# Performance work log

Hardware: AMD Instinct MI355X
Metric: run time of the kernel (lower is better)

Reference implementation:

```python
import jax, jax.numpy as jnp
import numpy as np

B = 4; C = 768; M = 6; P = 4
VIT = ((32, 32),)                      # ViT token grid (H//16, W//16) for a 512x512 image
PYR = ((64, 64), (32, 32), (16, 16))   # c2/c3/c4 pyramid levels
HID = 192                              # int(768 * cffn_ratio=0.25)


def _ln(x, g, b, eps=1e-6):
    mu = jnp.mean(x, -1, keepdims=True)
    var = jnp.mean((x - mu) ** 2, -1, keepdims=True)
    return (x - mu) * jax.lax.rsqrt(var + eps) * g + b


def _ref_points(shapes):
    # matches get_reference_points: centers of each cell, normalized to [0,1], (x, y) order
    refs = []
    for H, W in shapes:
        gy, gx = jnp.meshgrid((jnp.arange(H) + 0.5) / H, (jnp.arange(W) + 0.5) / W, indexing='ij')
        refs.append(jnp.stack([gx.reshape(-1), gy.reshape(-1)], -1))
    return jnp.concatenate(refs, 0)  # (N, 2)


def _bilinear(v, loc, H, W):
    # v: (B, M, H*W, Dh); loc: (B, Nq, M, P, 2) normalized to [0,1]
    # grid_sample semantics: align_corners=False, zero padding
    Bn, Mn, _, Dh = v.shape
    x = loc[..., 0] * W - 0.5
    y = loc[..., 1] * H - 0.5
    x0 = jnp.floor(x); y0 = jnp.floor(y)
    wx = x - x0; wy = y - y0

    def corner(xi, yi, w):
        valid = ((xi >= 0) & (xi < W) & (yi >= 0) & (yi < H)).astype(v.dtype)
        idx = (jnp.clip(yi, 0, H - 1) * W + jnp.clip(xi, 0, W - 1)).astype(jnp.int32)
        idx = jnp.transpose(idx, (0, 2, 1, 3)).reshape(Bn, Mn, -1)        # (B,M,Nq*P)
        g = jnp.take_along_axis(v, idx[..., None], axis=2)                # (B,M,Nq*P,Dh)
        wt = jnp.transpose(w * valid, (0, 2, 1, 3)).reshape(Bn, Mn, -1)
        return g * wt[..., None]

    return (corner(x0, y0, (1 - wx) * (1 - wy)) + corner(x0 + 1, y0, wx * (1 - wy))
            + corner(x0, y0 + 1, (1 - wx) * wy) + corner(x0 + 1, y0 + 1, wx * wy))


def _msda(q, kv, shapes, ref, ow, ob, aww, awb, vw, vb, pw, pb):
    # Multi-scale deformable attention (MSDeformAttn), proj_ratio=1.0
    Bn, Nq, Cd = q.shape
    L = len(shapes); Dh = Cd // M
    v = kv @ vw + vb                                                      # (B,S,C)
    offs = (q @ ow + ob).reshape(Bn, Nq, M, L, P, 2)
    aw = jax.nn.softmax((q @ aww + awb).reshape(Bn, Nq, M, L * P), -1).reshape(Bn, Nq, M, L, P)
    norm = jnp.asarray([[W, H] for (H, W) in shapes], dtype=q.dtype)      # (L,2), (W,H) order
    locs = ref[None, :, None, None, None, :] + offs / norm[None, None, None, :, None, :]
    out = jnp.zeros((Bn, Nq, M, Dh), q.dtype)
    s = 0
    for l, (H, W) in enumerate(shapes):
        n = H * W
        vl = v[:, s:s + n].reshape(Bn, n, M, Dh).transpose(0, 2, 1, 3)    # (B,M,n,Dh)
        s += n
        g = _bilinear(vl, locs[:, :, :, l], H, W).reshape(Bn, M, Nq, P, Dh)
        out = out + jnp.einsum('bmqpd,bqmp->bqmd', g, aw[:, :, :, l])
    return out.reshape(Bn, Nq, Cd) @ pw + pb


def _conv_ffn(cn, w1, b1, dw, db, w2, b2):
    h = cn @ w1 + b1                                                      # (B,N,HID)
    Bn = cn.shape[0]
    parts = []; s = 0
    for H, W in PYR:
        n = H * W
        seg = h[:, s:s + n].transpose(0, 2, 1).reshape(Bn, HID, H, W)
        seg = jax.lax.conv_general_dilated(seg, dw, (1, 1), 'SAME', feature_group_count=HID)
        seg = seg + db[None, :, None, None]
        parts.append(seg.reshape(Bn, HID, n).transpose(0, 2, 1))
        s += n
    h = jax.nn.gelu(jnp.concatenate(parts, 1), approximate=False)
    return h @ w2 + b2


def setup_inputs() -> dict:
    key = jax.random.key(0)
    ks = iter(jax.random.split(key, 64))

    def rn(*shape, s=0.02):
        return jax.random.normal(next(ks), shape, jnp.float32) * s

    Nvit = 32 * 32
    Npyr = 64 * 64 + 32 * 32 + 16 * 16
    d = {}
    d['x'] = jax.random.normal(next(ks), (B, Nvit, C), jnp.float32)
    d['c'] = jax.random.normal(next(ks), (B, Npyr, C), jnp.float32)
    for pre, L in (('inj', 3), ('ext', 1)):
        d[pre + '_n1g'] = jnp.ones((C,), jnp.float32); d[pre + '_n1b'] = jnp.zeros((C,), jnp.float32)
        d[pre + '_n2g'] = jnp.ones((C,), jnp.float32); d[pre + '_n2b'] = jnp.zeros((C,), jnp.float32)
        d[pre + '_off_w'] = rn(C, M * L * P * 2); d[pre + '_off_b'] = rn(M * L * P * 2, s=0.5)
        d[pre + '_aw_w'] = rn(C, M * L * P); d[pre + '_aw_b'] = jnp.zeros((M * L * P,), jnp.float32)
        d[pre + '_val_w'] = rn(C, C); d[pre + '_val_b'] = jnp.zeros((C,), jnp.float32)
        d[pre + '_out_w'] = rn(C, C); d[pre + '_out_b'] = jnp.zeros((C,), jnp.float32)
    d['inj_gamma'] = rn(C, s=0.1)
    d['ext_ng'] = jnp.ones((C,), jnp.float32); d['ext_nb'] = jnp.zeros((C,), jnp.float32)
    d['ext_fc1_w'] = rn(C, HID); d['ext_fc1_b'] = jnp.zeros((HID,), jnp.float32)
    d['ext_dw_w'] = rn(HID, 1, 3, 3, s=0.1); d['ext_dw_b'] = jnp.zeros((HID,), jnp.float32)
    d['ext_fc2_w'] = rn(HID, C); d['ext_fc2_b'] = jnp.zeros((C,), jnp.float32)
    return d


def reference(x, c, inj_n1g, inj_n1b, inj_n2g, inj_n2b, inj_off_w, inj_off_b, inj_aw_w, inj_aw_b,
              inj_val_w, inj_val_b, inj_out_w, inj_out_b, ext_n1g, ext_n1b, ext_n2g, ext_n2b,
              ext_off_w, ext_off_b, ext_aw_w, ext_aw_b, ext_val_w, ext_val_b, ext_out_w, ext_out_b,
              inj_gamma, ext_ng, ext_nb, ext_fc1_w, ext_fc1_b, ext_dw_w, ext_dw_b, ext_fc2_w, ext_fc2_b):
    ref_inj = _ref_points(VIT)   # queries = ViT tokens, kv = 3-level pyramid
    ref_ext = _ref_points(PYR)   # queries = pyramid tokens, kv = ViT grid (1 level)
    # Injector: x = x + gamma * MSDeformAttn(norm(x), ref, norm(c))
    attn = _msda(_ln(x, inj_n1g, inj_n1b), _ln(c, inj_n2g, inj_n2b), PYR, ref_inj,
                 inj_off_w, inj_off_b, inj_aw_w, inj_aw_b, inj_val_w, inj_val_b, inj_out_w, inj_out_b)
    x = x + inj_gamma * attn
    # Extractor: c = c + MSDeformAttn(norm(c), ref, norm(x)); c = c + ConvFFN(norm(c))
    attn = _msda(_ln(c, ext_n1g, ext_n1b), _ln(x, ext_n2g, ext_n2b), VIT, ref_ext,
                 ext_off_w, ext_off_b, ext_aw_w, ext_aw_b, ext_val_w, ext_val_b, ext_out_w, ext_out_b)
    c = c + attn
    c = c + _conv_ffn(_ln(c, ext_ng, ext_nb), ext_fc1_w, ext_fc1_b, ext_dw_w, ext_dw_b, ext_fc2_w, ext_fc2_b)
    return (x, c)
```

## Files before the change

kernel.cpp:

```cpp
#include <hip/hip_runtime.h>
#include <math.h>
#include <stdint.h>

#define CD 768
#define DH 128
#define MH 6

using half_t = _Float16;
typedef __attribute__((ext_vector_type(8))) _Float16 f16x8;
typedef __attribute__((ext_vector_type(4))) float f32x4;

__device__ __forceinline__ void gload16(const half_t* g, half_t* l) {
  __builtin_amdgcn_global_load_lds((__attribute__((address_space(1))) void*)g,
                                   (__attribute__((address_space(3))) void*)l, 16, 0, 0);
}

static __device__ __forceinline__ float wred(float v) {
#pragma unroll
  for (int off = 32; off > 0; off >>= 1) v += __shfl_down(v, off, 64);
  return v;
}

__global__ __launch_bounds__(256) void ln_f16(const float* __restrict__ in,
                                              const float* __restrict__ g,
                                              const float* __restrict__ b,
                                              half_t* __restrict__ out) {
  int row = blockIdx.x;
  const float* xp = in + (size_t)row * CD;
  half_t* op = out + (size_t)row * CD;
  int t = threadIdx.x;
  float v0 = xp[t], v1 = xp[t + 256], v2 = xp[t + 512];
  __shared__ float wsum[4];
  __shared__ float stat[2];
  int wid = t >> 6, lane = t & 63;
  float s = wred(v0 + v1 + v2);
  if (lane == 0) wsum[wid] = s;
  __syncthreads();
  if (t == 0) stat[0] = (wsum[0] + wsum[1] + wsum[2] + wsum[3]) * (1.0f / 768.0f);
  __syncthreads();
  float mu = stat[0];
  float d0 = v0 - mu, d1 = v1 - mu, d2 = v2 - mu;
  float q = wred(d0 * d0 + d1 * d1 + d2 * d2);
  if (lane == 0) wsum[wid] = q;
  __syncthreads();
  if (t == 0) {
    float var = (wsum[0] + wsum[1] + wsum[2] + wsum[3]) * (1.0f / 768.0f);
    stat[1] = 1.0f / sqrtf(var + 1e-6f);
  }
  __syncthreads();
  float rstd = stat[1];
  op[t]       = (half_t)(d0 * rstd * g[t]       + b[t]);
  op[t + 256] = (half_t)(d1 * rstd * g[t + 256] + b[t + 256]);
  op[t + 512] = (half_t)(d2 * rstd * g[t + 512] + b[t + 512]);
}

__global__ __launch_bounds__(256) void ln_dual(const float* __restrict__ in,
                                               const float* __restrict__ g1,
                                               const float* __restrict__ b1,
                                               half_t* __restrict__ o1,
                                               const float* __restrict__ g2,
                                               const float* __restrict__ b2,
                                               half_t* __restrict__ o2) {
  int row = blockIdx.x;
  const float* xp = in + (size_t)row * CD;
  int t = threadIdx.x;
  float v0 = xp[t], v1 = xp[t + 256], v2 = xp[t + 512];
  __shared__ float wsum[4];
  __shared__ float stat[2];
  int wid = t >> 6, lane = t & 63;
  float s = wred(v0 + v1 + v2);
  if (lane == 0) wsum[wid] = s;
  __syncthreads();
  if (t == 0) stat[0] = (wsum[0] + wsum[1] + wsum[2] + wsum[3]) * (1.0f / 768.0f);
  __syncthreads();
  float mu = stat[0];
  float d0 = v0 - mu, d1 = v1 - mu, d2 = v2 - mu;
  float q = wred(d0 * d0 + d1 * d1 + d2 * d2);
  if (lane == 0) wsum[wid] = q;
  __syncthreads();
  if (t == 0) {
    float var = (wsum[0] + wsum[1] + wsum[2] + wsum[3]) * (1.0f / 768.0f);
    stat[1] = 1.0f / sqrtf(var + 1e-6f);
  }
  __syncthreads();
  float rstd = stat[1];
  half_t* p1 = o1 + (size_t)row * CD;
  half_t* p2 = o2 + (size_t)row * CD;
  float n0 = d0 * rstd, n1 = d1 * rstd, n2 = d2 * rstd;
  p1[t]       = (half_t)(n0 * g1[t]       + b1[t]);
  p1[t + 256] = (half_t)(n1 * g1[t + 256] + b1[t + 256]);
  p1[t + 512] = (half_t)(n2 * g1[t + 512] + b1[t + 512]);
  p2[t]       = (half_t)(n0 * g2[t]       + b2[t]);
  p2[t + 256] = (half_t)(n1 * g2[t + 256] + b2[t + 256]);
  p2[t + 512] = (half_t)(n2 * g2[t + 512] + b2[t + 512]);
}

struct ConvArgs {
  const float* W[10];
  half_t* Wt[10];
  int K[10];
  int N[10];
  int base[11];
};
__global__ __launch_bounds__(256) void convert_all(ConvArgs a) {
  int idx = blockIdx.x * 256 + threadIdx.x;
  if (idx >= a.base[10]) return;
  int s = 0;
  while (idx >= a.base[s + 1]) ++s;
  int local = idx - a.base[s];
  int K = a.K[s], N = a.N[s];
  int n = local / K, k = local - n * K;
  a.Wt[s][local] = (n < N) ? (half_t)a.W[s][(size_t)k * N + n] : (half_t)0.0f;
}

template <int MODE, int OUTF16>
__global__ __launch_bounds__(256) void gemm_mfma(const half_t* __restrict__ A,
                                                 const half_t* __restrict__ Wt,
                                                 const float* __restrict__ bias,
                                                 const float* __restrict__ res,
                                                 const float* __restrict__ gamma,
                                                 void* __restrict__ outv,
                                                 int M, int N, int K) {
  __shared__ half_t smem[8192];
  const int tid = threadIdx.x;
  const int w = tid >> 6;
  const int l = tid & 63;
  const int wr = w >> 1, wc = w & 1;
  const int bm = blockIdx.y * 128;
  const int bn = blockIdx.x * 128;

  f32x4 acc[4][4];
#pragma unroll
  for (int i = 0; i < 4; ++i)
#pragma unroll
    for (int j = 0; j < 4; ++j) acc[i][j] = (f32x4){0.f, 0.f, 0.f, 0.f};

  const int j0 = w * 2;
  const int sr = l >> 2;
  const int sc = (l & 3) * 8;
  const half_t* Ag0 = A + (size_t)(bm + j0 * 16 + sr) * K + sc;
  const half_t* Ag1 = Ag0 + (size_t)16 * K;
  const half_t* Bg0 = Wt + (size_t)(bn + j0 * 16 + sr) * K + sc;
  const half_t* Bg1 = Bg0 + (size_t)16 * K;
  half_t* As0 = smem + j0 * 512;
  half_t* As1 = As0 + 512;
  half_t* Bs0 = smem + 4096 + j0 * 512;
  half_t* Bs1 = Bs0 + 512;

  const int fr = l & 15;
  const int fk = (l >> 4) * 8;
  const int abase = (wr * 64 + fr) * 32 + fk;
  const int bbase = 4096 + (wc * 64 + fr) * 32 + fk;

  for (int k0 = 0; k0 < K; k0 += 32) {
    gload16(Ag0 + k0, As0);
    gload16(Ag1 + k0, As1);
    gload16(Bg0 + k0, Bs0);
    gload16(Bg1 + k0, Bs1);
    __syncthreads();
    f16x8 af[4], bf[4];
#pragma unroll
    for (int i = 0; i < 4; ++i) {
      af[i] = *(const f16x8*)&smem[abase + i * 512];
      bf[i] = *(const f16x8*)&smem[bbase + i * 512];
    }
#pragma unroll
    for (int i = 0; i < 4; ++i)
#pragma unroll
      for (int j = 0; j < 4; ++j)
        acc[i][j] = __builtin_amdgcn_mfma_f32_16x16x32_f16(af[i], bf[j], acc[i][j], 0, 0, 0);
    __syncthreads();
  }

#pragma unroll
  for (int i = 0; i < 4; ++i) {
    int row0 = bm + wr * 64 + i * 16 + (l >> 4) * 4;
#pragma unroll
    for (int r = 0; r < 4; ++r) {
      size_t rowoff = (size_t)(row0 + r) * N;
#pragma unroll
      for (int j = 0; j < 4; ++j) {
        int col = bn + wc * 64 + j * 16 + fr;
        if (col < N) {
          float v = acc[i][j][r] + bias[col];
          if (MODE == 1) v = res[rowoff + col] + gamma[col] * v;
          else if (MODE == 2) v = res[rowoff + col] + v;
          if (OUTF16) ((half_t*)outv)[rowoff + col] = (half_t)v;
          else ((float*)outv)[rowoff + col] = v;
        }
      }
    }
  }
}

__global__ void softmax_lp(float* __restrict__ a, int total, int LP) {
  int i = blockIdx.x * blockDim.x + threadIdx.x;
  if (i >= total) return;
  float* p = a + (size_t)i * LP;
  float mx = -1e30f;
  for (int j = 0; j < LP; ++j) mx = fmaxf(mx, p[j]);
  float s = 0.0f;
  for (int j = 0; j < LP; ++j) {
    float e = expf(p[j] - mx);
    p[j] = e;
    s += e;
  }
  float inv = 1.0f / s;
  for (int j = 0; j < LP; ++j) p[j] *= inv;
}

__global__ __launch_bounds__(256) void sample_inj2(const half_t* __restrict__ v,
                                                   const float* __restrict__ offs,
                                                   const float* __restrict__ aw,
                                                   half_t* __restrict__ out) {
  int tid = threadIdx.x;
  int gp = blockIdx.x * 16 + (tid >> 4);
  int lane16 = tid & 15;
  int m = gp % MH;
  int bq = gp / MH;
  int q = bq & 1023;
  int b = bq >> 10;
  float refx = ((q & 31) + 0.5f) * (1.0f / 32.0f);
  float refy = ((q >> 5) + 0.5f) * (1.0f / 32.0f);
  const float* op = offs + (size_t)gp * 24;
  const float* ap = aw + (size_t)gp * 12;
  const half_t* vb = v + (size_t)b * 5376 * CD + m * DH + lane16 * 8;
  const int Hs[3] = {64, 32, 16};
  const int Ss[3] = {0, 4096, 5120};
  float accf[8];
#pragma unroll
  for (int i = 0; i < 8; ++i) accf[i] = 0.f;
#pragma unroll
  for (int lvl = 0; lvl < 3; ++lvl) {
    int H = Hs[lvl];
    float fH = (float)H;
    const half_t* vl = vb + (size_t)Ss[lvl] * CD;
#pragma unroll
    for (int p = 0; p < 4; ++p) {
      float xx = refx * fH + op[(lvl * 4 + p) * 2 + 0] - 0.5f;
      float yy = refy * fH + op[(lvl * 4 + p) * 2 + 1] - 0.5f;
      float x0f = floorf(xx), y0f = floorf(yy);
      float wx = xx - x0f, wy = yy - y0f;
      int x0 = (int)x0f, y0 = (int)y0f;
      float a = ap[lvl * 4 + p];
      f16x8 acch = (f16x8)(half_t)0.0f;
#pragma unroll
      for (int cy = 0; cy < 2; ++cy)
#pragma unroll
        for (int cx = 0; cx < 2; ++cx) {
          int xi = x0 + cx, yi = y0 + cy;
          bool valid = (xi >= 0) & (xi < H) & (yi >= 0) & (yi < H);
          float wgt = (cx ? wx : 1.f - wx) * (cy ? wy : 1.f - wy) * a;
          int xs = min(max(xi, 0), H - 1), ys = min(max(yi, 0), H - 1);
          half_t wch = (half_t)(valid ? wgt : 0.f);
          f16x8 vv = *(const f16x8*)(vl + (size_t)(ys * H + xs) * CD);
          acch += vv * wch;
        }
#pragma unroll
      for (int i = 0; i < 8; ++i) accf[i] += (float)acch[i];
    }
  }
  f16x8 r;
#pragma unroll
  for (int i = 0; i < 8; ++i) r[i] = (half_t)accf[i];
  *(f16x8*)(out + (size_t)bq * CD + m * DH + lane16 * 8) = r;
}

__global__ __launch_bounds__(256) void sample_ext2(const half_t* __restrict__ v,
                                                   const float* __restrict__ offs,
                                                   const float* __restrict__ aw,
                                                   half_t* __restrict__ out) {
  int tid = threadIdx.x;
  int gp = blockIdx.x * 16 + (tid >> 4);
  int lane16 = tid & 15;
  int m = gp % MH;
  int bq = gp / MH;
  int q = bq % 5376;
  int b = bq / 5376;
  float refx, refy;
  if (q < 4096) {
    refx = ((q & 63) + 0.5f) * (1.0f / 64.0f);
    refy = ((q >> 6) + 0.5f) * (1.0f / 64.0f);
  } else if (q < 5120) {
    int li = q - 4096;
    refx = ((li & 31) + 0.5f) * (1.0f / 32.0f);
    refy = ((li >> 5) + 0.5f) * (1.0f / 32.0f);
  } else {
    int li = q - 5120;
    refx = ((li & 15) + 0.5f) * (1.0f / 16.0f);
    refy = ((li >> 4) + 0.5f) * (1.0f / 16.0f);
  }
  const float* op = offs + (size_t)gp * 8;
  const float* ap = aw + (size_t)gp * 4;
  const half_t* vb = v + (size_t)b * 1024 * CD + m * DH + lane16 * 8;
  float accf[8];
#pragma unroll
  for (int i = 0; i < 8; ++i) accf[i] = 0.f;
#pragma unroll
  for (int p = 0; p < 4; ++p) {
    float xx = refx * 32.0f + op[p * 2 + 0] - 0.5f;
    float yy = refy * 32.0f + op[p * 2 + 1] - 0.5f;
    float x0f = floorf(xx), y0f = floorf(yy);
    float wx = xx - x0f, wy = yy - y0f;
    int x0 = (int)x0f, y0 = (int)y0f;
    float a = ap[p];
    f16x8 acch = (f16x8)(half_t)0.0f;
#pragma unroll
    for (int cy = 0; cy < 2; ++cy)
#pragma unroll
      for (int cx = 0; cx < 2; ++cx) {
        int xi = x0 + cx, yi = y0 + cy;
        bool valid = (xi >= 0) & (xi < 32) & (yi >= 0) & (yi < 32);
        float wgt = (cx ? wx : 1.f - wx) * (cy ? wy : 1.f - wy) * a;
        int xs = min(max(xi, 0), 31), ys = min(max(yi, 0), 31);
        half_t wch = (half_t)(valid ? wgt : 0.f);
        f16x8 vv = *(const f16x8*)(vb + (size_t)(ys * 32 + xs) * CD);
        acch += vv * wch;
      }
#pragma unroll
    for (int i = 0; i < 8; ++i) accf[i] += (float)acch[i];
  }
  f16x8 r;
#pragma unroll
  for (int i = 0; i < 8; ++i) r[i] = (half_t)accf[i];
  *(f16x8*)(out + (size_t)bq * CD + m * DH + lane16 * 8) = r;
}

__global__ __launch_bounds__(192) void dwconv_gelu(const half_t* __restrict__ h,
                                                   const float* __restrict__ w,
                                                   const float* __restrict__ bias,
                                                   half_t* __restrict__ out) {
  int bt = blockIdx.x;
  int tok = bt % 5376;
  int b = bt / 5376;
  int c = threadIdx.x;
  int H, s, li;
  if (tok < 4096) { H = 64; s = 0; li = tok; }
  else if (tok < 5120) { H = 32; s = 4096; li = tok - 4096; }
  else { H = 16; s = 5120; li = tok - 5120; }
  int y = li / H, x = li % H;
  const half_t* hb = h + ((size_t)b * 5376 + s) * 192 + c;
  float acc = 0.0f;
#pragma unroll
  for (int dy = -1; dy <= 1; ++dy) {
    int yy = y + dy;
    if (yy < 0 || yy >= H) continue;
#pragma unroll
    for (int dx = -1; dx <= 1; ++dx) {
      int xx = x + dx;
      if (xx < 0 || xx >= H) continue;
      acc += w[c * 9 + (dy + 1) * 3 + (dx + 1)] * (float)hb[(size_t)(yy * H + xx) * 192];
    }
  }
  acc += bias[c];
  float g = 0.5f * acc * (1.0f + erff(acc * 0.70710678118654752f));
  out[((size_t)b * 5376 + tok) * 192 + c] = (half_t)g;
}

extern "C" void kernel_launch(void* const* d_in, const int* in_sizes, int n_in,
                              void* d_out, int out_size, void* d_ws, size_t ws_size,
                              hipStream_t stream) {
  (void)in_sizes; (void)n_in; (void)out_size; (void)ws_size;
  const float* x        = (const float*)d_in[0];
  const float* c        = (const float*)d_in[1];
  const float* inj_n1g  = (const float*)d_in[2];
  const float* inj_n1b  = (const float*)d_in[3];
  const float* inj_n2g  = (const float*)d_in[4];
  const float* inj_n2b  = (const float*)d_in[5];
  const float* inj_off_w = (const float*)d_in[6];
  const float* inj_off_b = (const float*)d_in[7];
  const float* inj_aw_w = (const float*)d_in[8];
  const float* inj_aw_b = (const float*)d_in[9];
  const float* inj_val_w = (const float*)d_in[10];
  const float* inj_val_b = (const float*)d_in[11];
  const float* inj_out_w = (const float*)d_in[12];
  const float* inj_out_b = (const float*)d_in[13];
  const float* ext_n1g  = (const float*)d_in[14];
  const float* ext_n1b  = (const float*)d_in[15];
  const float* ext_n2g  = (const float*)d_in[16];
  const float* ext_n2b  = (const float*)d_in[17];
  const float* ext_off_w = (const float*)d_in[18];
  const float* ext_off_b = (const float*)d_in[19];
  const float* ext_aw_w = (const float*)d_in[20];
  const float* ext_aw_b = (const float*)d_in[21];
  const float* ext_val_w = (const float*)d_in[22];
  const float* ext_val_b = (const float*)d_in[23];
  const float* ext_out_w = (const float*)d_in[24];
  const float* ext_out_b = (const float*)d_in[25];
  const float* inj_gamma = (const float*)d_in[26];
  const float* ext_ng   = (const float*)d_in[27];
  const float* ext_nb   = (const float*)d_in[28];
  const float* ext_fc1_w = (const float*)d_in[29];
  const float* ext_fc1_b = (const float*)d_in[30];
  const float* ext_dw_w = (const float*)d_in[31];
  const float* ext_dw_b = (const float*)d_in[32];
  const float* ext_fc2_w = (const float*)d_in[33];
  const float* ext_fc2_b = (const float*)d_in[34];

  const int Sx = 4096;
  const int Sc = 21504;
  float* xout = (float*)d_out;
  float* cout = (float*)d_out + (size_t)Sx * CD;

  half_t* bigA   = (half_t*)d_ws;
  half_t* bigA2  = bigA + 16515072;
  half_t* bigV   = bigA2 + 16515072;
  half_t* smallA = bigV + 16515072;
  half_t* smallB = smallA + 3145728;
  half_t* h16    = smallB + 3145728;
  half_t* h2     = h16 + 4128768;
  half_t* w_inj_val = h2 + 4128768;
  half_t* w_inj_out = w_inj_val + 589824;
  half_t* w_ext_val = w_inj_out + 589824;
  half_t* w_ext_out = w_ext_val + 589824;
  half_t* w_fc2     = w_ext_out + 589824;
  half_t* w_inj_off = w_fc2 + 147456;
  half_t* w_inj_aw  = w_inj_off + 196608;
  half_t* w_ext_off = w_inj_aw + 98304;
  half_t* w_ext_aw  = w_ext_off + 98304;
  half_t* w_fc1     = w_ext_aw + 98304;
  float* offsb = (float*)(((uintptr_t)(w_fc1 + 196608) + 255) & ~(uintptr_t)255);
  float* awb = offsb + 1032192;

  ConvArgs ca;
  const float* srcs[10] = {inj_val_w, inj_off_w, inj_aw_w, inj_out_w, ext_val_w,
                           ext_off_w, ext_aw_w, ext_out_w, ext_fc1_w, ext_fc2_w};
  half_t* dsts[10] = {w_inj_val, w_inj_off, w_inj_aw, w_inj_out, w_ext_val,
                      w_ext_off, w_ext_aw, w_ext_out, w_fc1, w_fc2};
  int Ks[10]    = {768, 768, 768, 768, 768, 768, 768, 768, 768, 192};
  int Ns[10]    = {768, 144, 72, 768, 768, 48, 24, 768, 192, 768};
  int Npads[10] = {768, 256, 128, 768, 768, 128, 128, 768, 256, 768};
  int base = 0;
  for (int i = 0; i < 10; ++i) {
    ca.W[i] = srcs[i]; ca.Wt[i] = dsts[i]; ca.K[i] = Ks[i]; ca.N[i] = Ns[i];
    ca.base[i] = base; base += Npads[i] * Ks[i];
  }
  ca.base[10] = base;
  convert_all<<<(base + 255) / 256, 256, 0, stream>>>(ca);

  ln_f16<<<Sx, 256, 0, stream>>>(x, inj_n1g, inj_n1b, smallA);
  ln_dual<<<Sc, 256, 0, stream>>>(c, inj_n2g, inj_n2b, bigA, ext_n1g, ext_n1b, bigA2);
  gemm_mfma<0, 1><<<dim3(6, 168), 256, 0, stream>>>(bigA, w_inj_val, inj_val_b, nullptr, nullptr, bigV, Sc, 768, 768);
  gemm_mfma<0, 0><<<dim3(2, 32), 256, 0, stream>>>(smallA, w_inj_off, inj_off_b, nullptr, nullptr, offsb, Sx, 144, 768);
  gemm_mfma<0, 0><<<dim3(1, 32), 256, 0, stream>>>(smallA, w_inj_aw, inj_aw_b, nullptr, nullptr, awb, Sx, 72, 768);
  softmax_lp<<<(Sx * MH + 255) / 256, 256, 0, stream>>>(awb, Sx * MH, 12);
  sample_inj2<<<(Sx * MH) / 16, 256, 0, stream>>>(bigV, offsb, awb, smallB);
  gemm_mfma<1, 0><<<dim3(6, 32), 256, 0, stream>>>(smallB, w_inj_out, inj_out_b, x, inj_gamma, xout, Sx, 768, 768);

  ln_f16<<<Sx, 256, 0, stream>>>(xout, ext_n2g, ext_n2b, smallA);
  gemm_mfma<0, 1><<<dim3(6, 32), 256, 0, stream>>>(smallA, w_ext_val, ext_val_b, nullptr, nullptr, smallB, Sx, 768, 768);
  gemm_mfma<0, 0><<<dim3(1, 168), 256, 0, stream>>>(bigA2, w_ext_off, ext_off_b, nullptr, nullptr, offsb, Sc, 48, 768);
  gemm_mfma<0, 0><<<dim3(1, 168), 256, 0, stream>>>(bigA2, w_ext_aw, ext_aw_b, nullptr, nullptr, awb, Sc, 24, 768);
  softmax_lp<<<(Sc * MH + 255) / 256, 256, 0, stream>>>(awb, Sc * MH, 4);
  sample_ext2<<<(Sc * MH) / 16, 256, 0, stream>>>(smallB, offsb, awb, bigV);
  gemm_mfma<2, 0><<<dim3(6, 168), 256, 0, stream>>>(bigV, w_ext_out, ext_out_b, c, nullptr, cout, Sc, 768, 768);

  ln_f16<<<Sc, 256, 0, stream>>>(cout, ext_ng, ext_nb, bigA);
  gemm_mfma<0, 1><<<dim3(2, 168), 256, 0, stream>>>(bigA, w_fc1, ext_fc1_b, nullptr, nullptr, h16, Sc, 192, 768);
  dwconv_gelu<<<Sc, 192, 0, stream>>>(h16, ext_dw_w, ext_dw_b, h2);
  gemm_mfma<2, 0><<<dim3(6, 168), 256, 0, stream>>>(h2, w_fc2, ext_fc2_b, cout, nullptr, cout, Sc, 768, 192);
}
```

Measured before the change: 780.0 us.

## Double-buffer GEMM LDS loads, add XCD-aware tile swizzle, vectorize dwconv

The MFMA GEMM now uses two LDS buffers, issuing the next K-tile's global-to-LDS loads before computing on the current tile, so load latency can overlap with MFMA work. Workgroup indices are remapped so that blocks landing on the same XCD process contiguous output tiles, which is meant to improve L2 reuse. The depthwise conv+GELU kernel now processes 8 channels per thread with 16-byte vector loads and stores. The cost is doubled LDS use per block, which may reduce occupancy.

```diff
diff --git a/kernel.cpp b/kernel.cpp
--- a/kernel.cpp
+++ b/kernel.cpp
@@ -121,13 +121,19 @@
                                                  const float* __restrict__ gamma,
                                                  void* __restrict__ outv,
                                                  int M, int N, int K) {
-  __shared__ half_t smem[8192];
+  __shared__ half_t smem[16384];
   const int tid = threadIdx.x;
   const int w = tid >> 6;
   const int l = tid & 63;
   const int wr = w >> 1, wc = w & 1;
-  const int bm = blockIdx.y * 128;
-  const int bn = blockIdx.x * 128;
+
+  const int nwg = gridDim.x * gridDim.y;
+  const int orig = blockIdx.x + blockIdx.y * gridDim.x;
+  const int qq = nwg >> 3, rr = nwg & 7;
+  const int xcd = orig & 7, idx8 = orig >> 3;
+  const int sw = ((xcd < rr) ? xcd * (qq + 1) : rr * (qq + 1) + (xcd - rr) * qq) + idx8;
+  const int bm = (sw / gridDim.x) * 128;
+  const int bn = (sw % gridDim.x) * 128;
 
   f32x4 acc[4][4];
 #pragma unroll
@@ -142,27 +148,32 @@
   const half_t* Ag1 = Ag0 + (size_t)16 * K;
   const half_t* Bg0 = Wt + (size_t)(bn + j0 * 16 + sr) * K + sc;
   const half_t* Bg1 = Bg0 + (size_t)16 * K;
-  half_t* As0 = smem + j0 * 512;
-  half_t* As1 = As0 + 512;
-  half_t* Bs0 = smem + 4096 + j0 * 512;
-  half_t* Bs1 = Bs0 + 512;
 
   const int fr = l & 15;
   const int fk = (l >> 4) * 8;
   const int abase = (wr * 64 + fr) * 32 + fk;
   const int bbase = 4096 + (wc * 64 + fr) * 32 + fk;
 
-  for (int k0 = 0; k0 < K; k0 += 32) {
-    gload16(Ag0 + k0, As0);
-    gload16(Ag1 + k0, As1);
-    gload16(Bg0 + k0, Bs0);
-    gload16(Bg1 + k0, Bs1);
-    __syncthreads();
+  auto STAGE = [&](int buf, int k0) {
+    half_t* base = smem + buf * 8192;
+    gload16(Ag0 + k0, base + j0 * 512);
+    gload16(Ag1 + k0, base + j0 * 512 + 512);
+    gload16(Bg0 + k0, base + 4096 + j0 * 512);
+    gload16(Bg1 + k0, base + 4096 + j0 * 512 + 512);
+  };
+
+  const int NT = K >> 5;
+  STAGE(0, 0);
+  __syncthreads();
+  int cur = 0;
+  for (int t = 0; t < NT; ++t) {
+    if (t + 1 < NT) STAGE(cur ^ 1, (t + 1) << 5);
+    const half_t* rb = smem + cur * 8192;
     f16x8 af[4], bf[4];
 #pragma unroll
     for (int i = 0; i < 4; ++i) {
-      af[i] = *(const f16x8*)&smem[abase + i * 512];
-      bf[i] = *(const f16x8*)&smem[bbase + i * 512];
+      af[i] = *(const f16x8*)&rb[abase + i * 512];
+      bf[i] = *(const f16x8*)&rb[bbase + i * 512];
     }
 #pragma unroll
     for (int i = 0; i < 4; ++i)
@@ -170,6 +181,7 @@
       for (int j = 0; j < 4; ++j)
         acc[i][j] = __builtin_amdgcn_mfma_f32_16x16x32_f16(af[i], bf[j], acc[i][j], 0, 0, 0);
     __syncthreads();
+    cur ^= 1;
   }
 
 #pragma unroll
@@ -326,21 +338,25 @@
   *(f16x8*)(out + (size_t)bq * CD + m * DH + lane16 * 8) = r;
 }
 
-__global__ __launch_bounds__(192) void dwconv_gelu(const half_t* __restrict__ h,
+__global__ __launch_bounds__(256) void dwconv_gelu(const half_t* __restrict__ h,
                                                    const float* __restrict__ w,
                                                    const float* __restrict__ bias,
                                                    half_t* __restrict__ out) {
-  int bt = blockIdx.x;
-  int tok = bt % 5376;
-  int b = bt / 5376;
-  int c = threadIdx.x;
+  int g = blockIdx.x * 256 + threadIdx.x;
+  int cg = g % 24;
+  int tl = g / 24;
+  int tok = tl % 5376;
+  int b = tl / 5376;
   int H, s, li;
   if (tok < 4096) { H = 64; s = 0; li = tok; }
   else if (tok < 5120) { H = 32; s = 4096; li = tok - 4096; }
   else { H = 16; s = 5120; li = tok - 5120; }
   int y = li / H, x = li % H;
-  const half_t* hb = h + ((size_t)b * 5376 + s) * 192 + c;
-  float acc = 0.0f;
+  int c0 = cg * 8;
+  const half_t* hb = h + ((size_t)b * 5376 + s) * 192 + c0;
+  float acc[8];
+#pragma unroll
+  for (int i = 0; i < 8; ++i) acc[i] = bias[c0 + i];
 #pragma unroll
   for (int dy = -1; dy <= 1; ++dy) {
     int yy = y + dy;
@@ -349,12 +365,17 @@
     for (int dx = -1; dx <= 1; ++dx) {
       int xx = x + dx;
       if (xx < 0 || xx >= H) continue;
-      acc += w[c * 9 + (dy + 1) * 3 + (dx + 1)] * (float)hb[(size_t)(yy * H + xx) * 192];
+      int k = (dy + 1) * 3 + (dx + 1);
+      f16x8 vv = *(const f16x8*)(hb + (size_t)(yy * H + xx) * 192);
+#pragma unroll
+      for (int i = 0; i < 8; ++i) acc[i] += w[(c0 + i) * 9 + k] * (float)vv[i];
     }
   }
-  acc += bias[c];
-  float g = 0.5f * acc * (1.0f + erff(acc * 0.70710678118654752f));
-  out[((size_t)b * 5376 + tok) * 192 + c] = (half_t)g;
+  f16x8 r;
+#pragma unroll
+  for (int i = 0; i < 8; ++i)
+    r[i] = (half_t)(0.5f * acc[i] * (1.0f + erff(acc[i] * 0.70710678118654752f)));
+  *(f16x8*)(out + (size_t)tl * 192 + c0) = r;
 }
 
 extern "C" void kernel_launch(void* const* d_in, const int* in_sizes, int n_in,
@@ -457,6 +478,6 @@
 
   ln_f16<<<Sc, 256, 0, stream>>>(cout, ext_ng, ext_nb, bigA);
   gemm_mfma<0, 1><<<dim3(2, 168), 256, 0, stream>>>(bigA, w_fc1, ext_fc1_b, nullptr, nullptr, h16, Sc, 192, 768);
-  dwconv_gelu<<<Sc, 192, 0, stream>>>(h16, ext_dw_w, ext_dw_b, h2);
+  dwconv_gelu<<<(Sc * 24) / 256, 256, 0, stream>>>(h16, ext_dw_w, ext_dw_b, h2);
   gemm_mfma<2, 0><<<dim3(6, 168), 256, 0, stream>>>(h2, w_fc2, ext_fc2_b, cout, nullptr, cout, Sc, 768, 192);
 }
```

New measurement: 754.0 us. 3.3% less time.
